# Kernel optimization log

Measured on AMD Instinct MI355X. Metric: run time of the kernel, lower is better.

## Reference

```python
import jax, jax.numpy as jnp
import numpy as np
import math

B, S, D, H, L, DFF, V = 4, 1024, 512, 8, 4, 2048, 32000
DK = D // H
SPARSITY = 0.3
K = max(1, int(S * SPARSITY))  # 307
EPS = 1e-5


def _layernorm(x, g, b):
    mu = jnp.mean(x, axis=-1, keepdims=True)
    var = jnp.mean(jnp.square(x - mu), axis=-1, keepdims=True)
    return (x - mu) * jax.lax.rsqrt(var + EPS) * g + b


def _scatter_topk(scores, k):
    # scores: [B,H,S,S]. keep top-k per row, others -inf (torch.topk + scatter_)
    vals, idx = jax.lax.top_k(scores, k)
    lead = int(np.prod(scores.shape[:-1]))
    sk = scores.shape[-1]
    sparse = jnp.full((lead, sk), -jnp.inf, dtype=scores.dtype)
    rows = jnp.arange(lead)[:, None]
    sparse = sparse.at[rows, idx.reshape(lead, k)].set(vals.reshape(lead, k))
    return sparse.reshape(scores.shape)


def _forward(x, tok_emb, pos_emb, Wq, bq, Wk, bk, Wv, bv, Wo, bo,
             g1, be1, g2, be2, W1, b1, Wm, bm, W2, b2, Wout, bout):
    h = tok_emb[x] + pos_emb[jnp.arange(S)][None, :, :]  # [B,S,D]
    scale = 1.0 / math.sqrt(DK)
    for l in range(L):
        y = _layernorm(h, g1[l], be1[l])
        q = (y @ Wq[l] + bq[l]).reshape(B, S, H, DK).transpose(0, 2, 1, 3)
        kk = (y @ Wk[l] + bk[l]).reshape(B, S, H, DK).transpose(0, 2, 1, 3)
        v = (y @ Wv[l] + bv[l]).reshape(B, S, H, DK).transpose(0, 2, 1, 3)
        scores = jnp.einsum('bhqd,bhkd->bhqk', q, kk) * scale
        sparse = _scatter_topk(scores, K)
        attn = jax.nn.softmax(sparse, axis=-1)
        o = jnp.einsum('bhqk,bhkd->bhqd', attn, v)
        o = o.transpose(0, 2, 1, 3).reshape(B, S, D) @ Wo[l] + bo[l]
        h = h + o
        z = _layernorm(h, g2[l], be2[l])
        f = jax.nn.gelu(z @ W1[l] + b1[l], approximate=False)
        f = jax.nn.gelu(f @ Wm[l] + bm[l], approximate=False)
        f = f @ W2[l] + b2[l]
        h = h + f
    return h @ Wout + bout  # logits [B,S,V]


def setup_inputs() -> dict:
    key = jax.random.key(0)
    ks = iter(jax.random.split(key, 32))
    xa = lambda shape, fan: (jax.random.normal(next(ks), shape, jnp.float32)
                             * math.sqrt(2.0 / fan))
    return {
        'x': jax.random.randint(next(ks), (B, S), 0, V, dtype=jnp.int32),
        'tok_emb': xa((V, D), V + D),
        'pos_emb': xa((S, D), S + D),
        'Wq': xa((L, D, D), 2 * D), 'bq': jnp.zeros((L, D), jnp.float32),
        'Wk': xa((L, D, D), 2 * D), 'bk': jnp.zeros((L, D), jnp.float32),
        'Wv': xa((L, D, D), 2 * D), 'bv': jnp.zeros((L, D), jnp.float32),
        'Wo': xa((L, D, D), 2 * D), 'bo': jnp.zeros((L, D), jnp.float32),
        'g1': jnp.ones((L, D), jnp.float32), 'be1': jnp.zeros((L, D), jnp.float32),
        'g2': jnp.ones((L, D), jnp.float32), 'be2': jnp.zeros((L, D), jnp.float32),
        'W1': xa((L, D, DFF), D + DFF), 'b1': jnp.zeros((L, DFF), jnp.float32),
        'Wm': xa((L, DFF, DFF), 2 * DFF), 'bm': jnp.zeros((L, DFF), jnp.float32),
        'W2': xa((L, DFF, D), D + DFF), 'b2': jnp.zeros((L, D), jnp.float32),
        'Wout': xa((D, V), D + V), 'bout': jnp.zeros((V,), jnp.float32),
    }


def reference(x, tok_emb, pos_emb, Wq, bq, Wk, bk, Wv, bv, Wo, bo,
              g1, be1, g2, be2, W1, b1, Wm, bm, W2, b2, Wout, bout):
    return _forward(x, tok_emb, pos_emb, Wq, bq, Wk, bk, Wv, bv, Wo, bo,
                    g1, be1, g2, be2, W1, b1, Wm, bm, W2, b2, Wout, bout)
```

## Files before the change

### kernel.cpp

```cpp
#include <hip/hip_runtime.h>
#include <hip/hip_bf16.h>
#include <math.h>

#define B_ 4
#define S_ 1024
#define D_ 512
#define H_ 8
#define L_ 4
#define DFF_ 2048
#define V_ 32000
#define DK_ 64
#define KTOP 307
#define SRS 1048

using bf16x8 = __attribute__((ext_vector_type(8))) __bf16;
using bf16x4 = __attribute__((ext_vector_type(4))) __bf16;
using bf16x2 = __attribute__((ext_vector_type(2))) __bf16;
using f32x4v = __attribute__((ext_vector_type(4))) float;

__device__ __forceinline__ void gload_lds16(const __bf16* g, __bf16* l) {
  __builtin_amdgcn_global_load_lds(
      (const __attribute__((address_space(1))) void*)g,
      (__attribute__((address_space(3))) void*)l, 16, 0, 0);
}

__device__ __forceinline__ unsigned int f32_to_bf16_bits(float s) {
  unsigned int x = __float_as_uint(s);
  return (x + 0x7FFFu + ((x >> 16) & 1u)) >> 16;
}

template<int ROWS>
__device__ __forceinline__ void stage_tile4(const __bf16* src, int Kd, __bf16* lds,
                                            int w, int lane) {
  #pragma unroll
  for (int c = 0; c < ROWS / 32; ++c) {
    int rblk = (c * 4 + w) * 8;
    int row = rblk + (lane >> 3);
    int col = (lane & 7) * 8;
    int scol = col ^ ((row & 4) ? 16 : 0);
    gload_lds16(src + (size_t)row * Kd + scol, lds + rblk * 64);
  }
}
__device__ __forceinline__ void stage_half8(const __bf16* src, int Kd, __bf16* lds,
                                            int w, int lane) {
  #pragma unroll
  for (int c = 0; c < 2; ++c) {
    int rblk = (c * 8 + w) * 8;
    int row = rblk + (lane >> 3);
    int col = (lane & 7) * 8;
    int scol = col ^ ((row & 4) ? 16 : 0);
    gload_lds16(src + (size_t)row * Kd + scol, lds + rblk * 64);
  }
}
__device__ __forceinline__ bf16x8 lds_frag64(const __bf16* lds, int row, int colbase) {
  int col = colbase ^ ((row & 4) ? 16 : 0);
  return *reinterpret_cast<const bf16x8*>(lds + row * 64 + col);
}

__global__ void embed_kernel(const int* __restrict__ x, const float* __restrict__ tok,
                             const float* __restrict__ pos, float* __restrict__ h) {
  int row = blockIdx.x;
  int t = threadIdx.x;
  int s = row & (S_ - 1);
  int token = x[row];
  const float4* t4 = reinterpret_cast<const float4*>(tok + (size_t)token * D_);
  const float4* p4 = reinterpret_cast<const float4*>(pos + (size_t)s * D_);
  float4 a = t4[t];
  float4 b = p4[t];
  a.x += b.x; a.y += b.y; a.z += b.z; a.w += b.w;
  reinterpret_cast<float4*>(h + (size_t)row * D_)[t] = a;
}

__global__ void ln_kernel(const float* __restrict__ xin, const float* __restrict__ g,
                          const float* __restrict__ bta, __bf16* __restrict__ y) {
  int row = blockIdx.x;
  int t = threadIdx.x;
  const float2* x2 = reinterpret_cast<const float2*>(xin + (size_t)row * D_);
  float2 v = x2[t];
  float s = v.x + v.y;
  #pragma unroll
  for (int m = 1; m < 64; m <<= 1) s += __shfl_xor(s, m, 64);
  __shared__ float red[4];
  __shared__ float red2[4];
  int wid = t >> 6, lane = t & 63;
  if (lane == 0) red[wid] = s;
  __syncthreads();
  float mu = (red[0] + red[1] + red[2] + red[3]) * (1.0f / D_);
  float dx = v.x - mu, dy = v.y - mu;
  float s2 = dx * dx + dy * dy;
  #pragma unroll
  for (int m = 1; m < 64; m <<= 1) s2 += __shfl_xor(s2, m, 64);
  if (lane == 0) red2[wid] = s2;
  __syncthreads();
  float var = (red2[0] + red2[1] + red2[2] + red2[3]) * (1.0f / D_);
  float rstd = rsqrtf(var + 1e-5f);
  float2 gg = reinterpret_cast<const float2*>(g)[t];
  float2 bb = reinterpret_cast<const float2*>(bta)[t];
  bf16x2 o2;
  o2[0] = (__bf16)(dx * rstd * gg.x + bb.x);
  o2[1] = (__bf16)(dy * rstd * gg.y + bb.y);
  *reinterpret_cast<bf16x2*>(y + (size_t)row * D_ + t * 2) = o2;
}

__global__ void transpose_bf16_kernel(const float* __restrict__ in, __bf16* __restrict__ out,
                                      int Kd, int N, long in_bstride, long out_bstride) {
  __shared__ float tile[32][33];
  const float* ib = in + (size_t)blockIdx.z * in_bstride;
  __bf16* ob = out + (size_t)blockIdx.z * out_bstride;
  int n0 = blockIdx.x * 32, k0 = blockIdx.y * 32;
  int tx = threadIdx.x & 31, ty = threadIdx.x >> 5;
  #pragma unroll
  for (int i = 0; i < 4; ++i)
    tile[ty + i * 8][tx] = ib[(size_t)(k0 + ty + i * 8) * N + n0 + tx];
  __syncthreads();
  #pragma unroll
  for (int i = 0; i < 4; ++i)
    ob[(size_t)(n0 + ty + i * 8) * Kd + k0 + tx] = (__bf16)tile[tx][ty + i * 8];
}

__global__ void concat_bias_kernel(const float* __restrict__ bq, const float* __restrict__ bk,
                                   const float* __restrict__ bv, float* __restrict__ bqkv) {
  int i = blockIdx.x * 256 + threadIdx.x;
  int l = i / 1536, c = i - l * 1536;
  float v = (c < 512) ? bq[l * 512 + c]
          : (c < 1024) ? bk[l * 512 + c - 512]
                       : bv[l * 512 + c - 1024];
  bqkv[i] = v;
}

#define BM 128
#define BN 128
#define BK 64

template<int OMODE, bool GELU_ACT, bool RES, bool SWZ>
__global__ __launch_bounds__(256)
void gemm_bf16_kernel(const __bf16* __restrict__ A, const __bf16* __restrict__ WT,
                      const float* __restrict__ bias, const float* __restrict__ res,
                      void* __restrict__ outp, void* __restrict__ outp2, void* __restrict__ outp3,
                      int M, int N, int Kd) {
  __shared__ __bf16 As[BM * BK];
  __shared__ __bf16 Ws[BN * BK];
  int tid = threadIdx.x;
  int lane = tid & 63, w = tid >> 6;
  int wr = w >> 1, wc = w & 1;
  int lr = lane & 15, lg = lane >> 4;
  int bx, by;
  if (SWZ) {
    int lid = blockIdx.x;
    int cpx = gridDim.x >> 3;
    int swz = (lid & 7) * cpx + (lid >> 3);
    int gx = M >> 7;
    bx = swz % gx;
    by = swz / gx;
  } else {
    bx = blockIdx.x; by = blockIdx.y;
  }
  int row0 = bx * BM, col0 = by * BN;

  const __bf16* Abase = A + (size_t)row0 * Kd;
  const __bf16* Wbase = WT + (size_t)col0 * Kd;

  f32x4v acc[4][4];
  #pragma unroll
  for (int i = 0; i < 4; ++i)
    #pragma unroll
    for (int j = 0; j < 4; ++j)
      #pragma unroll
      for (int e = 0; e < 4; ++e) acc[i][j][e] = 0.0f;

  for (int k0 = 0; k0 < Kd; k0 += BK) {
    stage_tile4<128>(Abase + k0, Kd, As, w, lane);
    stage_tile4<128>(Wbase + k0, Kd, Ws, w, lane);
    __syncthreads();
    bf16x8 af[4][2], bfr[4][2];
    #pragma unroll
    for (int mr = 0; mr < 4; ++mr)
      #pragma unroll
      for (int kk = 0; kk < 2; ++kk)
        af[mr][kk] = lds_frag64(As, wr * 64 + mr * 16 + lr, kk * 32 + lg * 8);
    #pragma unroll
    for (int nc = 0; nc < 4; ++nc)
      #pragma unroll
      for (int kk = 0; kk < 2; ++kk)
        bfr[nc][kk] = lds_frag64(Ws, wc * 64 + nc * 16 + lr, kk * 32 + lg * 8);
    __builtin_amdgcn_s_setprio(1);
    #pragma unroll
    for (int mr = 0; mr < 4; ++mr)
      #pragma unroll
      for (int nc = 0; nc < 4; ++nc) {
        acc[mr][nc] = __builtin_amdgcn_mfma_f32_16x16x32_bf16(af[mr][0], bfr[nc][0], acc[mr][nc], 0, 0, 0);
        acc[mr][nc] = __builtin_amdgcn_mfma_f32_16x16x32_bf16(af[mr][1], bfr[nc][1], acc[mr][nc], 0, 0, 0);
      }
    __builtin_amdgcn_s_setprio(0);
    __syncthreads();
  }

  #pragma unroll
  for (int mr = 0; mr < 4; ++mr) {
    #pragma unroll
    for (int nc = 0; nc < 4; ++nc) {
      int c = col0 + wc * 64 + nc * 16 + lr;
      int rb = row0 + wr * 64 + mr * 16 + lg * 4;
      float vv[4];
      #pragma unroll
      for (int j = 0; j < 4; ++j) {
        float t = acc[mr][nc][j] + bias[c];
        if (RES) t += res[(size_t)(rb + j) * N + c];
        if (GELU_ACT) t = 0.5f * t * (1.0f + erff(t * 0.70710678118654752f));
        vv[j] = t;
      }
      if (OMODE == 0) {
        float* out = (float*)outp;
        #pragma unroll
        for (int j = 0; j < 4; ++j) out[(size_t)(rb + j) * N + c] = vv[j];
      } else if (OMODE == 1) {
        __bf16* out = (__bf16*)outp;
        #pragma unroll
        for (int j = 0; j < 4; ++j) out[(size_t)(rb + j) * N + c] = (__bf16)vv[j];
      } else if (OMODE == 3) {
        float* out = (float*)outp;
        __bf16* out2 = (__bf16*)outp2;
        #pragma unroll
        for (int j = 0; j < 4; ++j) {
          out[(size_t)(rb + j) * N + c] = vv[j];
          out2[(size_t)(rb + j) * N + c] = (__bf16)vv[j];
        }
      } else {
        if (col0 < 512) {
          __bf16* out = (__bf16*)outp;
          #pragma unroll
          for (int j = 0; j < 4; ++j) out[(size_t)(rb + j) * D_ + c] = (__bf16)vv[j];
        } else if (col0 < 1024) {
          __bf16* out = (__bf16*)outp2;
          #pragma unroll
          for (int j = 0; j < 4; ++j) out[(size_t)(rb + j) * D_ + (c - 512)] = (__bf16)vv[j];
        } else {
          __bf16* out = (__bf16*)outp3;
          int b = rb >> 10, s0 = rb & (S_ - 1);
          bf16x4 pk;
          #pragma unroll
          for (int j = 0; j < 4; ++j) pk[j] = (__bf16)vv[j];
          *reinterpret_cast<bf16x4*>(&out[((size_t)b * D_ + (c - 1024)) * S_ + s0]) = pk;
        }
      }
    }
  }
}

template<int OMODE, bool RES>
__global__ __launch_bounds__(256)
void gemm64_kernel(const __bf16* __restrict__ A, const __bf16* __restrict__ WT,
                   const float* __restrict__ bias, const float* __restrict__ res,
                   void* __restrict__ outp, void* __restrict__ outp2,
                   int M, int N, int Kd) {
  __shared__ __bf16 As[64 * BK];
  __shared__ __bf16 Ws[BN * BK];
  int tid = threadIdx.x;
  int lane = tid & 63, w = tid >> 6;
  int wr = w >> 1, wc = w & 1;
  int lr = lane & 15, lg = lane >> 4;
  int row0 = blockIdx.x * 64, col0 = blockIdx.y * BN;

  const __bf16* Abase = A + (size_t)row0 * Kd;
  const __bf16* Wbase = WT + (size_t)col0 * Kd;

  f32x4v acc[2][4];
  #pragma unroll
  for (int i = 0; i < 2; ++i)
    #pragma unroll
    for (int j = 0; j < 4; ++j)
      #pragma unroll
      for (int e = 0; e < 4; ++e) acc[i][j][e] = 0.0f;

  for (int k0 = 0; k0 < Kd; k0 += BK) {
    stage_tile4<64>(Abase + k0, Kd, As, w, lane);
    stage_tile4<128>(Wbase + k0, Kd, Ws, w, lane);
    __syncthreads();
    bf16x8 af[2][2], bfr[4][2];
    #pragma unroll
    for (int mr = 0; mr < 2; ++mr)
      #pragma unroll
      for (int kk = 0; kk < 2; ++kk)
        af[mr][kk] = lds_frag64(As, wr * 32 + mr * 16 + lr, kk * 32 + lg * 8);
    #pragma unroll
    for (int nc = 0; nc < 4; ++nc)
      #pragma unroll
      for (int kk = 0; kk < 2; ++kk)
        bfr[nc][kk] = lds_frag64(Ws, wc * 64 + nc * 16 + lr, kk * 32 + lg * 8);
    __builtin_amdgcn_s_setprio(1);
    #pragma unroll
    for (int mr = 0; mr < 2; ++mr)
      #pragma unroll
      for (int nc = 0; nc < 4; ++nc) {
        acc[mr][nc] = __builtin_amdgcn_mfma_f32_16x16x32_bf16(af[mr][0], bfr[nc][0], acc[mr][nc], 0, 0, 0);
        acc[mr][nc] = __builtin_amdgcn_mfma_f32_16x16x32_bf16(af[mr][1], bfr[nc][1], acc[mr][nc], 0, 0, 0);
      }
    __builtin_amdgcn_s_setprio(0);
    __syncthreads();
  }

  #pragma unroll
  for (int mr = 0; mr < 2; ++mr) {
    #pragma unroll
    for (int nc = 0; nc < 4; ++nc) {
      int c = col0 + wc * 64 + nc * 16 + lr;
      int rb = row0 + wr * 32 + mr * 16 + lg * 4;
      float vv[4];
      #pragma unroll
      for (int j = 0; j < 4; ++j) {
        float t = acc[mr][nc][j] + bias[c];
        if (RES) t += res[(size_t)(rb + j) * N + c];
        vv[j] = t;
      }
      if (OMODE == 0) {
        float* out = (float*)outp;
        #pragma unroll
        for (int j = 0; j < 4; ++j) out[(size_t)(rb + j) * N + c] = vv[j];
      } else {
        float* out = (float*)outp;
        __bf16* out2 = (__bf16*)outp2;
        #pragma unroll
        for (int j = 0; j < 4; ++j) {
          out[(size_t)(rb + j) * N + c] = vv[j];
          out2[(size_t)(rb + j) * N + c] = (__bf16)vv[j];
        }
      }
    }
  }
}

__global__ __launch_bounds__(512)
void gemm_head_kernel(const __bf16* __restrict__ A, const __bf16* __restrict__ WT,
                      const float* __restrict__ bias, float* __restrict__ out,
                      int M, int N, int Kd) {
  __shared__ __bf16 lds[2][2][256 * 64];
  const int tid = threadIdx.x;
  const int lane = tid & 63, w = tid >> 6;
  const int wr = w >> 2, wc = w & 3;
  const int lr = lane & 15, lg = lane >> 4;

  int lid = blockIdx.x;
  int cpx = gridDim.x >> 3;
  int swz = (lid & 7) * cpx + (lid >> 3);
  int gx = M >> 8;
  int bx = swz % gx, by = swz / gx;
  int row0 = bx * 256, col0 = by * 256;

  const __bf16* Asrc = A + (size_t)row0 * Kd;
  const __bf16* Bsrc = WT + (size_t)col0 * Kd;

  f32x4v acc[8][4];
  #pragma unroll
  for (int i = 0; i < 8; ++i)
    #pragma unroll
    for (int j = 0; j < 4; ++j)
      #pragma unroll
      for (int e = 0; e < 4; ++e) acc[i][j][e] = 0.0f;

  const int NT = Kd / 64;
  stage_half8(Asrc,                      Kd, &lds[0][0][0],    w, lane);
  stage_half8(Asrc + (size_t)128 * Kd,   Kd, &lds[0][0][8192], w, lane);
  stage_half8(Bsrc,                      Kd, &lds[0][1][0],    w, lane);
  stage_half8(Bsrc + (size_t)128 * Kd,   Kd, &lds[0][1][8192], w, lane);

  for (int t = 0; t < NT; ++t) {
    int cur = t & 1, nxt = cur ^ 1;
    int k1 = (t + 1) * 64;
    const __bf16* Ab = &lds[cur][0][0];
    const __bf16* Bb = &lds[cur][1][0];
    bf16x8 bfr[4][2];
    #pragma unroll
    for (int p = 0; p < 4; ++p) {
      if (t < NT - 1) {
        const __bf16* s;
        __bf16* d;
        if (p == 0)      { s = Asrc + k1;                    d = &lds[nxt][0][0]; }
        else if (p == 1) { s = Asrc + (size_t)128 * Kd + k1; d = &lds[nxt][0][8192]; }
        else if (p == 2) { s = Bsrc + k1;                    d = &lds[nxt][1][0]; }
        else             { s = Bsrc + (size_t)128 * Kd + k1; d = &lds[nxt][1][8192]; }
        stage_half8(s, Kd, d, w, lane);
      }
      if (p == 0) {
        if (t < NT - 1) asm volatile("s_waitcnt vmcnt(2)" ::: "memory");
        else            asm volatile("s_waitcnt vmcnt(0)" ::: "memory");
        __builtin_amdgcn_s_barrier();
        #pragma unroll
        for (int nn = 0; nn < 4; ++nn)
          #pragma unroll
          for (int kk = 0; kk < 2; ++kk)
            bfr[nn][kk] = lds_frag64(Bb, wc * 64 + nn * 16 + lr, kk * 32 + lg * 8);
      }
      bf16x8 af[2][2];
      #pragma unroll
      for (int mm = 0; mm < 2; ++mm)
        #pragma unroll
        for (int kk = 0; kk < 2; ++kk)
          af[mm][kk] = lds_frag64(Ab, wr * 128 + p * 32 + mm * 16 + lr, kk * 32 + lg * 8);
      asm volatile("s_waitcnt lgkmcnt(0)" ::: "memory");
      __builtin_amdgcn_sched_barrier(0);
      __builtin_amdgcn_s_setprio(1);
      #pragma unroll
      for (int mm = 0; mm < 2; ++mm)
        #pragma unroll
        for (int nn = 0; nn < 4; ++nn) {
          acc[p * 2 + mm][nn] = __builtin_amdgcn_mfma_f32_16x16x32_bf16(af[mm][0], bfr[nn][0], acc[p * 2 + mm][nn], 0, 0, 0);
          acc[p * 2 + mm][nn] = __builtin_amdgcn_mfma_f32_16x16x32_bf16(af[mm][1], bfr[nn][1], acc[p * 2 + mm][nn], 0, 0, 0);
        }
      __builtin_amdgcn_s_setprio(0);
    }
    __builtin_amdgcn_s_barrier();
  }

  #pragma unroll
  for (int mg = 0; mg < 8; ++mg) {
    #pragma unroll
    for (int nn = 0; nn < 4; ++nn) {
      int c = col0 + wc * 64 + nn * 16 + lr;
      int rb = row0 + wr * 128 + mg * 16 + lg * 4;
      float b = bias[c];
      #pragma unroll
      for (int j = 0; j < 4; ++j)
        out[(size_t)(rb + j) * N + c] = acc[mg][nn][j] + b;
    }
  }
}

__global__ __launch_bounds__(256)
void attn_kernel(const __bf16* __restrict__ qm, const __bf16* __restrict__ km,
                 const __bf16* __restrict__ vt, __bf16* __restrict__ o) {
  __shared__ unsigned short sc16[16][SRS];
  __shared__ float rs[16];
  const int q0 = blockIdx.x * 16;
  const int hh = blockIdx.y;
  const int bb = blockIdx.z;
  const int tid = threadIdx.x;
  const int lane = tid & 63, w = tid >> 6;
  const int lr = lane & 15, lg = lane >> 4;

  const __bf16* qrow = qm + ((size_t)(bb * S_ + q0 + lr)) * D_ + hh * DK_;
  bf16x8 qf0 = *reinterpret_cast<const bf16x8*>(qrow + lg * 8);
  bf16x8 qf1 = *reinterpret_cast<const bf16x8*>(qrow + 32 + lg * 8);

  const __bf16* kbase = km + ((size_t)bb * S_) * D_ + hh * DK_;
  #pragma unroll 4
  for (int kt = 0; kt < 16; ++kt) {
    int key0 = kt * 64 + w * 16;
    const __bf16* krow = kbase + (size_t)(key0 + lr) * D_;
    bf16x8 kf0 = *reinterpret_cast<const bf16x8*>(krow + lg * 8);
    bf16x8 kf1 = *reinterpret_cast<const bf16x8*>(krow + 32 + lg * 8);
    f32x4v d = {0.0f, 0.0f, 0.0f, 0.0f};
    __builtin_amdgcn_s_setprio(1);
    d = __builtin_amdgcn_mfma_f32_16x16x32_bf16(qf0, kf0, d, 0, 0, 0);
    d = __builtin_amdgcn_mfma_f32_16x16x32_bf16(qf1, kf1, d, 0, 0, 0);
    __builtin_amdgcn_s_setprio(0);
    #pragma unroll
    for (int j = 0; j < 4; ++j) {
      unsigned int u = f32_to_bf16_bits(d[j] * 0.125f);
      u = (u & 0x8000u) ? (~u & 0xFFFFu) : (u | 0x8000u);
      sc16[lg * 4 + j][key0 + lr] = (unsigned short)u;
    }
  }
  __syncthreads();

  {
    int r = tid >> 4, tc = tid & 15;
    const unsigned int* srow = reinterpret_cast<const unsigned int*>(&sc16[r][0]);
    unsigned int wv[32];
    #pragma unroll
    for (int g = 0; g < 8; ++g) {
      uint4 t4 = *reinterpret_cast<const uint4*>(&srow[g * 64 + tc * 4]);
      wv[g * 4 + 0] = t4.x; wv[g * 4 + 1] = t4.y;
      wv[g * 4 + 2] = t4.z; wv[g * 4 + 3] = t4.w;
    }
    unsigned int umax = 0;
    #pragma unroll
    for (int i = 0; i < 32; ++i) {
      unsigned int a = wv[i] & 0xFFFFu, b = wv[i] >> 16;
      unsigned int mx = a > b ? a : b;
      umax = mx > umax ? mx : umax;
    }
    #pragma unroll
    for (int m = 1; m < 16; m <<= 1) {
      unsigned int other = (unsigned int)__shfl_xor((int)umax, m, 64);
      umax = other > umax ? other : umax;
    }
    unsigned int lo = 0;
    for (int bit = 15; bit >= 0; --bit) {
      unsigned int cs = (lo | (1u << bit)) << 16;
      int cnt = 0;
      #pragma unroll
      for (int i = 0; i < 32; ++i) {
        cnt += ((wv[i] << 16) >= cs) ? 1 : 0;
        cnt += (wv[i] >= cs) ? 1 : 0;
      }
      #pragma unroll
      for (int m = 1; m < 16; m <<= 1) cnt += __shfl_xor(cnt, m, 64);
      if (cnt >= KTOP) lo |= (1u << bit);
    }
    unsigned int um = (umax & 0x8000u) ? (umax ^ 0x8000u) : (~umax & 0xFFFFu);
    float mval = __uint_as_float(um << 16);

    __bf16* P = reinterpret_cast<__bf16*>(&sc16[r][0]);
    float lsum = 0.0f;
    #pragma unroll
    for (int g = 0; g < 8; ++g) {
      bf16x8 pk;
      #pragma unroll
      for (int e = 0; e < 8; ++e) {
        unsigned int wrd = wv[g * 4 + (e >> 1)];
        unsigned int u = (e & 1) ? (wrd >> 16) : (wrd & 0xFFFFu);
        float p = 0.0f;
        if (u >= lo) {
          unsigned int ub = (u & 0x8000u) ? (u ^ 0x8000u) : (~u & 0xFFFFu);
          p = __expf(__uint_as_float(ub << 16) - mval);
        }
        pk[e] = (__bf16)p;
        lsum += (float)pk[e];
      }
      *reinterpret_cast<bf16x8*>(&P[tc * 8 + g * 128]) = pk;
    }
    #pragma unroll
    for (int m = 1; m < 16; m <<= 1) lsum += __shfl_xor(lsum, m, 64);
    if (tc == 0) rs[r] = lsum;
  }
  __syncthreads();

  {
    const __bf16* P0 = reinterpret_cast<const __bf16*>(&sc16[0][0]);
    const __bf16* vbase = vt + ((size_t)bb * D_ + hh * DK_ + w * 16 + lr) * S_;
    const __bf16* prow = P0 + (size_t)lr * SRS;
    f32x4v oacc = {0.0f, 0.0f, 0.0f, 0.0f};
    #pragma unroll 4
    for (int kt = 0; kt < 32; ++kt) {
      bf16x8 a = *reinterpret_cast<const bf16x8*>(prow + kt * 32 + lg * 8);
      bf16x8 b = *reinterpret_cast<const bf16x8*>(vbase + kt * 32 + lg * 8);
      __builtin_amdgcn_s_setprio(1);
      oacc = __builtin_amdgcn_mfma_f32_16x16x32_bf16(a, b, oacc, 0, 0, 0);
      __builtin_amdgcn_s_setprio(0);
    }
    #pragma unroll
    for (int j = 0; j < 4; ++j) {
      int qr = lg * 4 + j;
      float ov = oacc[j] / rs[qr];
      o[((size_t)(bb * S_ + q0 + qr)) * D_ + hh * DK_ + w * 16 + lr] = (__bf16)ov;
    }
  }
}

extern "C" void kernel_launch(void* const* d_in, const int* in_sizes, int n_in,
                              void* d_out, int out_size, void* d_ws, size_t ws_size,
                              hipStream_t stream) {
  (void)in_sizes; (void)n_in; (void)out_size; (void)ws_size;
  const int*   x    = (const int*)d_in[0];
  const float* tok  = (const float*)d_in[1];
  const float* pos  = (const float*)d_in[2];
  const float* Wq   = (const float*)d_in[3];
  const float* bq   = (const float*)d_in[4];
  const float* Wk   = (const float*)d_in[5];
  const float* bk   = (const float*)d_in[6];
  const float* Wv   = (const float*)d_in[7];
  const float* bv   = (const float*)d_in[8];
  const float* Wo   = (const float*)d_in[9];
  const float* bo   = (const float*)d_in[10];
  const float* g1   = (const float*)d_in[11];
  const float* be1  = (const float*)d_in[12];
  const float* g2   = (const float*)d_in[13];
  const float* be2  = (const float*)d_in[14];
  const float* W1   = (const float*)d_in[15];
  const float* b1   = (const float*)d_in[16];
  const float* Wm   = (const float*)d_in[17];
  const float* bm   = (const float*)d_in[18];
  const float* W2   = (const float*)d_in[19];
  const float* b2   = (const float*)d_in[20];
  const float* Wout = (const float*)d_in[21];
  const float* bout = (const float*)d_in[22];
  float* logits = (float*)d_out;

  const int M = B_ * S_;
  float* ws = (float*)d_ws;
  float* h    = ws;
  float* bqkv = h + (size_t)M * D_;
  __bf16* y16  = (__bf16*)(bqkv + (size_t)L_ * 1536);
  __bf16* f1b  = y16  + (size_t)M * D_;
  __bf16* f2b  = f1b  + (size_t)M * DFF_;
  __bf16* qb16 = f2b  + (size_t)M * DFF_;
  __bf16* kb16 = qb16 + (size_t)M * D_;
  __bf16* vt16 = kb16 + (size_t)M * D_;
  __bf16* ob16 = vt16 + (size_t)M * D_;
  __bf16* h16  = ob16 + (size_t)M * D_;
  __bf16* WqkvT = h16 + (size_t)M * D_;
  __bf16* WoT  = WqkvT + (size_t)L_ * 1536 * D_;
  __bf16* W1T  = WoT  + (size_t)L_ * D_ * D_;
  __bf16* WmT  = W1T  + (size_t)L_ * D_ * DFF_;
  __bf16* W2T  = WmT  + (size_t)L_ * DFF_ * DFF_;
  __bf16* WoutT = W2T + (size_t)L_ * D_ * DFF_;

  const long DD = (long)D_ * D_;
  transpose_bf16_kernel<<<dim3(D_/32,  D_/32,   L_), 256, 0, stream>>>(Wq, WqkvT,            D_, D_, DD, 1536L*D_);
  transpose_bf16_kernel<<<dim3(D_/32,  D_/32,   L_), 256, 0, stream>>>(Wk, WqkvT + 512*512,  D_, D_, DD, 1536L*D_);
  transpose_bf16_kernel<<<dim3(D_/32,  D_/32,   L_), 256, 0, stream>>>(Wv, WqkvT + 1024*512, D_, D_, DD, 1536L*D_);
  transpose_bf16_kernel<<<dim3(D_/32,  D_/32,   L_), 256, 0, stream>>>(Wo, WoT, D_, D_, DD, DD);
  transpose_bf16_kernel<<<dim3(DFF_/32, D_/32,  L_), 256, 0, stream>>>(W1, W1T, D_, DFF_, (long)D_*DFF_, (long)D_*DFF_);
  transpose_bf16_kernel<<<dim3(DFF_/32, DFF_/32,L_), 256, 0, stream>>>(Wm, WmT, DFF_, DFF_, (long)DFF_*DFF_, (long)DFF_*DFF_);
  transpose_bf16_kernel<<<dim3(D_/32,  DFF_/32, L_), 256, 0, stream>>>(W2, W2T, DFF_, D_, (long)D_*DFF_, (long)D_*DFF_);
  transpose_bf16_kernel<<<dim3(V_/32,  D_/32,   1 ), 256, 0, stream>>>(Wout, WoutT, D_, V_, (long)D_*V_, (long)D_*V_);
  concat_bias_kernel<<<(L_*1536)/256, 256, 0, stream>>>(bq, bk, bv, bqkv);

  embed_kernel<<<M, 128, 0, stream>>>(x, tok, pos, h);

  for (int l = 0; l < L_; ++l) {
    ln_kernel<<<M, 256, 0, stream>>>(h, g1 + l * D_, be1 + l * D_, y16);
    gemm_bf16_kernel<4,false,false,true><<<dim3((M/BM) * (1536/BN)), 256, 0, stream>>>(
        y16, WqkvT + (size_t)l * 1536 * D_, bqkv + l * 1536, nullptr,
        qb16, kb16, vt16, M, 1536, D_);
    attn_kernel<<<dim3(S_/16, H_, B_), 256, 0, stream>>>(qb16, kb16, vt16, ob16);
    gemm64_kernel<0,true><<<dim3(M/64, D_/BN), 256, 0, stream>>>(
        ob16, WoT + (size_t)l * DD, bo + l * D_, h, h, nullptr, M, D_, D_);
    ln_kernel<<<M, 256, 0, stream>>>(h, g2 + l * D_, be2 + l * D_, y16);
    gemm_bf16_kernel<1,true,false,true><<<dim3((M/BM) * (DFF_/BN)), 256, 0, stream>>>(
        y16, W1T + (size_t)l * D_ * DFF_, b1 + l * DFF_, nullptr, f1b, nullptr, nullptr, M, DFF_, D_);
    gemm_bf16_kernel<1,true,false,true><<<dim3((M/BM) * (DFF_/BN)), 256, 0, stream>>>(
        f1b, WmT + (size_t)l * DFF_ * DFF_, bm + l * DFF_, nullptr, f2b, nullptr, nullptr, M, DFF_, DFF_);
    gemm64_kernel<3,true><<<dim3(M/64, D_/BN), 256, 0, stream>>>(
        f2b, W2T + (size_t)l * D_ * DFF_, b2 + l * D_, h, h, h16, M, D_, DFF_);
  }
  gemm_head_kernel<<<dim3((M/256) * (V_/256)), 512, 0, stream>>>(
      h16, WoutT, bout, logits, M, V_, D_);
}
```

Before: 1.344 ms.

## Use DPP reductions, single-pass layernorm stats, and wider LDS swizzle

Replaces shuffle-based 16-lane reductions in the top-k attention kernel with DPP row operations, which avoid LDS-routed shuffles in the 16-step radix search loop. Layernorm now computes sum and sum of squares in one pass, removing one barrier and reduction round at the cost of a less numerically stable variance formula. The LDS XOR swizzle for 64-wide tiles changes from a single-bit pattern to a full 3-bit row-based pattern to reduce bank conflicts in the GEMM fragment loads.

Result: faster. 1.280 ms (-4.7%).

```diff
diff --git a/kernel.cpp b/kernel.cpp
--- a/kernel.cpp
+++ b/kernel.cpp
@@ -29,6 +29,35 @@
   return (x + 0x7FFFu + ((x >> 16) & 1u)) >> 16;
 }
 
+__device__ __forceinline__ int red16i(int x) {
+  x += __builtin_amdgcn_update_dpp(0, x, 0xB1, 0xF, 0xF, true);
+  x += __builtin_amdgcn_update_dpp(0, x, 0x4E, 0xF, 0xF, true);
+  x += __builtin_amdgcn_update_dpp(0, x, 0x141, 0xF, 0xF, true);
+  x += __builtin_amdgcn_update_dpp(0, x, 0x140, 0xF, 0xF, true);
+  return x;
+}
+__device__ __forceinline__ unsigned int red16umax(unsigned int x) {
+  unsigned int t;
+  t = (unsigned int)__builtin_amdgcn_update_dpp(0, (int)x, 0xB1, 0xF, 0xF, true);  x = t > x ? t : x;
+  t = (unsigned int)__builtin_amdgcn_update_dpp(0, (int)x, 0x4E, 0xF, 0xF, true);  x = t > x ? t : x;
+  t = (unsigned int)__builtin_amdgcn_update_dpp(0, (int)x, 0x141, 0xF, 0xF, true); x = t > x ? t : x;
+  t = (unsigned int)__builtin_amdgcn_update_dpp(0, (int)x, 0x140, 0xF, 0xF, true); x = t > x ? t : x;
+  return x;
+}
+__device__ __forceinline__ float red16f(float x) {
+  x += __int_as_float(__builtin_amdgcn_update_dpp(0, __float_as_int(x), 0xB1, 0xF, 0xF, true));
+  x += __int_as_float(__builtin_amdgcn_update_dpp(0, __float_as_int(x), 0x4E, 0xF, 0xF, true));
+  x += __int_as_float(__builtin_amdgcn_update_dpp(0, __float_as_int(x), 0x141, 0xF, 0xF, true));
+  x += __int_as_float(__builtin_amdgcn_update_dpp(0, __float_as_int(x), 0x140, 0xF, 0xF, true));
+  return x;
+}
+__device__ __forceinline__ float red64f(float x) {
+  x = red16f(x);
+  x += __shfl_xor(x, 16, 64);
+  x += __shfl_xor(x, 32, 64);
+  return x;
+}
+
 template<int ROWS>
 __device__ __forceinline__ void stage_tile4(const __bf16* src, int Kd, __bf16* lds,
                                             int w, int lane) {
@@ -37,7 +66,7 @@
     int rblk = (c * 4 + w) * 8;
     int row = rblk + (lane >> 3);
     int col = (lane & 7) * 8;
-    int scol = col ^ ((row & 4) ? 16 : 0);
+    int scol = col ^ ((row & 7) << 3);
     gload_lds16(src + (size_t)row * Kd + scol, lds + rblk * 64);
   }
 }
@@ -48,12 +77,12 @@
     int rblk = (c * 8 + w) * 8;
     int row = rblk + (lane >> 3);
     int col = (lane & 7) * 8;
-    int scol = col ^ ((row & 4) ? 16 : 0);
+    int scol = col ^ ((row & 7) << 3);
     gload_lds16(src + (size_t)row * Kd + scol, lds + rblk * 64);
   }
 }
 __device__ __forceinline__ bf16x8 lds_frag64(const __bf16* lds, int row, int colbase) {
-  int col = colbase ^ ((row & 4) ? 16 : 0);
+  int col = colbase ^ ((row & 7) << 3);
   return *reinterpret_cast<const bf16x8*>(lds + row * 64 + col);
 }
 
@@ -78,27 +107,23 @@
   const float2* x2 = reinterpret_cast<const float2*>(xin + (size_t)row * D_);
   float2 v = x2[t];
   float s = v.x + v.y;
-  #pragma unroll
-  for (int m = 1; m < 64; m <<= 1) s += __shfl_xor(s, m, 64);
+  float q = v.x * v.x + v.y * v.y;
+  s = red64f(s);
+  q = red64f(q);
   __shared__ float red[4];
   __shared__ float red2[4];
   int wid = t >> 6, lane = t & 63;
-  if (lane == 0) red[wid] = s;
+  if (lane == 0) { red[wid] = s; red2[wid] = q; }
   __syncthreads();
   float mu = (red[0] + red[1] + red[2] + red[3]) * (1.0f / D_);
-  float dx = v.x - mu, dy = v.y - mu;
-  float s2 = dx * dx + dy * dy;
-  #pragma unroll
-  for (int m = 1; m < 64; m <<= 1) s2 += __shfl_xor(s2, m, 64);
-  if (lane == 0) red2[wid] = s2;
-  __syncthreads();
-  float var = (red2[0] + red2[1] + red2[2] + red2[3]) * (1.0f / D_);
+  float ex2 = (red2[0] + red2[1] + red2[2] + red2[3]) * (1.0f / D_);
+  float var = ex2 - mu * mu;
   float rstd = rsqrtf(var + 1e-5f);
   float2 gg = reinterpret_cast<const float2*>(g)[t];
   float2 bb = reinterpret_cast<const float2*>(bta)[t];
   bf16x2 o2;
-  o2[0] = (__bf16)(dx * rstd * gg.x + bb.x);
-  o2[1] = (__bf16)(dy * rstd * gg.y + bb.y);
+  o2[0] = (__bf16)((v.x - mu) * rstd * gg.x + bb.x);
+  o2[1] = (__bf16)((v.y - mu) * rstd * gg.y + bb.y);
   *reinterpret_cast<bf16x2*>(y + (size_t)row * D_ + t * 2) = o2;
 }
 
@@ -479,11 +504,7 @@
       unsigned int mx = a > b ? a : b;
       umax = mx > umax ? mx : umax;
     }
-    #pragma unroll
-    for (int m = 1; m < 16; m <<= 1) {
-      unsigned int other = (unsigned int)__shfl_xor((int)umax, m, 64);
-      umax = other > umax ? other : umax;
-    }
+    umax = red16umax(umax);
     unsigned int lo = 0;
     for (int bit = 15; bit >= 0; --bit) {
       unsigned int cs = (lo | (1u << bit)) << 16;
@@ -493,8 +514,7 @@
         cnt += ((wv[i] << 16) >= cs) ? 1 : 0;
         cnt += (wv[i] >= cs) ? 1 : 0;
       }
-      #pragma unroll
-      for (int m = 1; m < 16; m <<= 1) cnt += __shfl_xor(cnt, m, 64);
+      cnt = red16i(cnt);
       if (cnt >= KTOP) lo |= (1u << bit);
     }
     unsigned int um = (umax & 0x8000u) ? (umax ^ 0x8000u) : (~umax & 0xFFFFu);
@@ -519,8 +539,7 @@
       }
       *reinterpret_cast<bf16x8*>(&P[tc * 8 + g * 128]) = pk;
     }
-    #pragma unroll
-    for (int m = 1; m < 16; m <<= 1) lsum += __shfl_xor(lsum, m, 64);
+    lsum = red16f(lsum);
     if (tc == 0) rs[r] = lsum;
   }
   __syncthreads();
```
